# Kernel tuning notes

Measured on AMD Instinct MI355X. Metric: run time of the kernel, lower is better.

The kernel has to match this reference:

```python
import jax, jax.numpy as jnp
import numpy as np

N_NODES = 100000
N_EDGES = 1600000
DIM = 64
BN_EPS = 1e-5


def setup_inputs() -> dict:
    key = jax.random.key(0)
    ks = jax.random.split(key, 6)
    x = jax.random.normal(ks[0], (N_NODES, DIM), dtype=jnp.float32)
    edge_index = jax.random.randint(ks[1], (2, N_EDGES), 0, N_NODES, dtype=jnp.int32)
    W = jax.random.normal(ks[2], (DIM, DIM), dtype=jnp.float32) / np.sqrt(DIM)
    b = jax.random.normal(ks[3], (DIM,), dtype=jnp.float32) * 0.01
    gamma = jnp.ones((DIM,), dtype=jnp.float32)
    beta = jnp.zeros((DIM,), dtype=jnp.float32)
    return {"x": x, "edge_index": edge_index, "W": W, "b": b, "gamma": gamma, "beta": beta}


def reference(x, edge_index, W, b, gamma, beta):
    n = x.shape[0]
    src, dst = edge_index[0], edge_index[1]
    # GCNConv adds self loops
    loop = jnp.arange(n, dtype=edge_index.dtype)
    src = jnp.concatenate([src, loop])
    dst = jnp.concatenate([dst, loop])
    # symmetric degree normalization: D^-1/2 (A+I) D^-1/2
    deg = jax.ops.segment_sum(jnp.ones(src.shape[0], x.dtype), dst, num_segments=n)
    dinv = jnp.where(deg > 0, jax.lax.rsqrt(deg), 0.0)
    norm = dinv[src] * dinv[dst]  # [E+N]
    h = x @ W  # [N, D] transform before aggregation (GCN order)
    msg = h[src] * norm[:, None]  # gather + scale
    out = jax.ops.segment_sum(msg, dst, num_segments=n) + b  # scatter-add
    # BatchNorm1d (training mode: batch statistics, biased variance)
    mean = jnp.mean(out, axis=0)
    var = jnp.mean(jnp.square(out - mean), axis=0)
    out = (out - mean) * jax.lax.rsqrt(var + BN_EPS) * gamma + beta
    # ReLU; dropout is identity in eval mode
    return jax.nn.relu(out)
```

## Files before the change

### kernel.cpp

```cpp
#include <hip/hip_runtime.h>

#define N_NODES 100000
#define N_EDGES 1600000
#define DIM 64
#define BN_EPS 1e-5f

#define BNODES 128
#define NBUCK ((N_NODES + BNODES - 1) / BNODES)
#define CAP_RAW 2560
#define CAP_OUT 3584
#define TILE 8192
#define ABLK ((N_EDGES + TILE - 1) / TILE)

#define GBLK 6250
#define NREP 32

typedef __bf16 bf16x8 __attribute__((ext_vector_type(8)));
typedef float floatx4 __attribute__((ext_vector_type(4)));

static __device__ __forceinline__ unsigned short f2bf(float f) {
    unsigned u = __float_as_uint(f);
    u = (u + 0x7FFFu + ((u >> 16) & 1u)) >> 16;
    return (unsigned short)u;
}
static __device__ __forceinline__ float bf2f(unsigned short h) {
    return __uint_as_float(((unsigned)h) << 16);
}

__global__ void __launch_bounds__(1024)
passA_kernel(const int* __restrict__ src, const int* __restrict__ dst,
             int* __restrict__ cur, unsigned int* __restrict__ entries, int E) {
    __shared__ int hist[NBUCK];
    __shared__ int lbase[NBUCK];
    int t = threadIdx.x;
    if (t < NBUCK) hist[t] = 0;
    __syncthreads();

    int e0   = blockIdx.x * TILE;
    int eend = min(e0 + TILE, E);
    int eb   = e0 + t * 8;

    int dreg[8], sreg[8], ne = 0;
    if (eb + 7 < eend) {
        int4 d4 = *(const int4*)(dst + eb);
        int4 s4 = *(const int4*)(src + eb);
        int4 d5 = *(const int4*)(dst + eb + 4);
        int4 s5 = *(const int4*)(src + eb + 4);
        dreg[0] = d4.x; dreg[1] = d4.y; dreg[2] = d4.z; dreg[3] = d4.w;
        sreg[0] = s4.x; sreg[1] = s4.y; sreg[2] = s4.z; sreg[3] = s4.w;
        dreg[4] = d5.x; dreg[5] = d5.y; dreg[6] = d5.z; dreg[7] = d5.w;
        sreg[4] = s5.x; sreg[5] = s5.y; sreg[6] = s5.z; sreg[7] = s5.w;
        ne = 8;
    } else {
        for (int e = eb; e < eend && ne < 8; ++e, ++ne) {
            dreg[ne] = dst[e];
            sreg[ne] = src[e];
        }
    }
#pragma unroll
    for (int k = 0; k < 8; ++k)
        if (k < ne) atomicAdd(&hist[dreg[k] >> 7], 1);
    __syncthreads();
    if (t < NBUCK) {
        int ii = t + (blockIdx.x * 331) % NBUCK;
        if (ii >= NBUCK) ii -= NBUCK;
        int c = hist[ii];
        lbase[ii] = (c > 0) ? atomicAdd(&cur[ii], c) : 0;
        hist[ii] = 0;
    }
    __syncthreads();
#pragma unroll
    for (int k = 0; k < 8; ++k) {
        if (k >= ne) break;
        int s = sreg[k];
        int d = dreg[k];
        int b = d >> 7;
        int r = atomicAdd(&hist[b], 1);
        int pos = lbase[b] + r;
        if (pos < CAP_RAW)
            entries[(size_t)b * CAP_OUT + pos] = ((unsigned)s << 7) | (unsigned)(d & 127);
    }
}

__global__ void __launch_bounds__(256)
build_kernel(unsigned int* __restrict__ entries, const int* __restrict__ cur,
             int* __restrict__ rowbeg, int* __restrict__ rowend,
             float* __restrict__ dinv,
             const float* __restrict__ x, const float* __restrict__ W,
             unsigned short* __restrict__ hb, int dummyIdx, int N) {
    __shared__ int hist[BNODES * 4];
    __shared__ int nstart[BNODES];
    __shared__ int cursor[BNODES * 4];
    __shared__ int w0tot;
    int bucket = blockIdx.x;
    int t = threadIdx.x;
    int lane = t & 63, wv = t >> 6;
    int node0 = bucket * BNODES;
    int nn = min(BNODES, N - node0);
    int cnt = min(cur[bucket], CAP_RAW);
    unsigned int* eb = entries + (size_t)bucket * CAP_OUT;

    int m = lane & 15, quad = lane >> 4;
    int nchunk = nn >> 4;
    bool vA = (wv < nchunk);
    bool vB = (wv + 4 < nchunk);
    int rowA = node0 + wv * 16 + m;
    int rowB = node0 + (wv + 4) * 16 + m;
    float4 xA[4], xB[4];
    if (vA) {
        const float* xr = x + (size_t)rowA * DIM;
#pragma unroll
        for (int c = 0; c < 2; ++c) {
            xA[c * 2]     = *(const float4*)(xr + c * 32 + quad * 8);
            xA[c * 2 + 1] = *(const float4*)(xr + c * 32 + quad * 8 + 4);
        }
    }
    if (vB) {
        const float* xr = x + (size_t)rowB * DIM;
#pragma unroll
        for (int c = 0; c < 2; ++c) {
            xB[c * 2]     = *(const float4*)(xr + c * 32 + quad * 8);
            xB[c * 2 + 1] = *(const float4*)(xr + c * 32 + quad * 8 + 4);
        }
    }

    for (int i = t; i < BNODES * 4; i += 256) hist[i] = 0;
    __syncthreads();

    unsigned int ereg[10];
#pragma unroll
    for (int k = 0; k < 10; ++k) {
        int i = t + k * 256;
        if (i < cnt) {
            unsigned int e = eb[i];
            ereg[k] = e;
            int s = (int)(e >> 7);
            int q = (s >= 25000) + (s >= 50000) + (s >= 75000);
            atomicAdd(&hist[((e & 127) << 2) | q], 1);
        }
    }

    bf16x8 bfrag[2][4];
#pragma unroll
    for (int c = 0; c < 2; ++c)
#pragma unroll
        for (int nt = 0; nt < 4; ++nt) {
            bf16x8 f;
#pragma unroll
            for (int j = 0; j < 8; ++j) {
                int k = c * 32 + quad * 8 + j;
                f[j] = (__bf16)W[k * DIM + nt * 16 + m];
            }
            bfrag[c][nt] = f;
        }
    __syncthreads();

    int lrowA = wv * 16 + m, lrowB = (wv + 4) * 16 + m;
    float dvA = rsqrtf((float)(1 + hist[lrowA * 4] + hist[lrowA * 4 + 1] +
                               hist[lrowA * 4 + 2] + hist[lrowA * 4 + 3]));
    float dvB = rsqrtf((float)(1 + hist[lrowB * 4] + hist[lrowB * 4 + 1] +
                               hist[lrowB * 4 + 2] + hist[lrowB * 4 + 3]));

    int deg_t = 0, pdeg_t = 0;
    if (t < BNODES) {
        deg_t = hist[t * 4] + hist[t * 4 + 1] + hist[t * 4 + 2] + hist[t * 4 + 3];
        pdeg_t = (deg_t + 7) & ~7;
    }
    int v = pdeg_t;
#pragma unroll
    for (int off = 1; off < 64; off <<= 1) {
        int u = __shfl_up(v, off, 64);
        if (lane >= off) v += u;
    }
    if (t == 63) w0tot = v;
    __syncthreads();
    if (t < BNODES) {
        int incl = v + (wv == 1 ? w0tot : 0);
        int ex = incl - pdeg_t;
        nstart[t] = ex;
        int o = ex;
        cursor[t * 4 + 0] = o; o += hist[t * 4 + 0];
        cursor[t * 4 + 1] = o; o += hist[t * 4 + 1];
        cursor[t * 4 + 2] = o; o += hist[t * 4 + 2];
        cursor[t * 4 + 3] = o;
    }
    __syncthreads();
#pragma unroll
    for (int k = 0; k < 10; ++k) {
        int i = t + k * 256;
        if (i < cnt) {
            unsigned int e = ereg[k];
            int s = (int)(e >> 7);
            int q = (s >= 25000) + (s >= 50000) + (s >= 75000);
            int p = atomicAdd(&cursor[((e & 127) << 2) | q], 1);
            eb[p] = (unsigned)s;
        }
    }
    if (t < nn) {
        int dg  = deg_t;
        int pdg = pdeg_t;
        int base = nstart[t];
        for (int k = dg; k < pdg; ++k) eb[base + k] = (unsigned)dummyIdx;
        int gbase = bucket * CAP_OUT + base;
        rowbeg[node0 + t] = gbase;
        rowend[node0 + t] = gbase + pdg;
        dinv[node0 + t] = rsqrtf((float)(dg + 1));
    }

#pragma unroll
    for (int slot = 0; slot < 2; ++slot) {
        bool valid = slot == 0 ? vA : vB;
        if (!valid) continue;
        int row = slot == 0 ? rowA : rowB;
        float dv = slot == 0 ? dvA : dvB;
        bf16x8 afrag[2];
#pragma unroll
        for (int c = 0; c < 2; ++c) {
            float4 lo = slot == 0 ? xA[c * 2] : xB[c * 2];
            float4 hi = slot == 0 ? xA[c * 2 + 1] : xB[c * 2 + 1];
            bf16x8 f;
            f[0] = (__bf16)lo.x; f[1] = (__bf16)lo.y; f[2] = (__bf16)lo.z; f[3] = (__bf16)lo.w;
            f[4] = (__bf16)hi.x; f[5] = (__bf16)hi.y; f[6] = (__bf16)hi.z; f[7] = (__bf16)hi.w;
            afrag[c] = f;
        }
#pragma unroll
        for (int nt = 0; nt < 4; ++nt) {
            floatx4 acc = {0.f, 0.f, 0.f, 0.f};
            acc = __builtin_amdgcn_mfma_f32_16x16x32_bf16(bfrag[0][nt], afrag[0], acc, 0, 0, 0);
            acc = __builtin_amdgcn_mfma_f32_16x16x32_bf16(bfrag[1][nt], afrag[1], acc, 0, 0, 0);
            ushort4 pk;
            pk.x = f2bf(acc[0] * dv);
            pk.y = f2bf(acc[1] * dv);
            pk.z = f2bf(acc[2] * dv);
            pk.w = f2bf(acc[3] * dv);
            *(ushort4*)(hb + (size_t)row * DIM + nt * 16 + quad * 4) = pk;
        }
    }
}

__global__ void __launch_bounds__(256)
gather_kernel(const int* __restrict__ rowbeg, const int* __restrict__ rowend,
              const unsigned int* __restrict__ srt, const unsigned short* __restrict__ hb,
              const float* __restrict__ dinv, unsigned short* __restrict__ hbout,
              float* __restrict__ gstatRep, int N) {
    __shared__ float red[2][4][64];
    int lane = threadIdx.x & 63;
    int wv   = threadIdx.x >> 6;
    int g    = blockIdx.x * 4 + wv;
    int n0   = g << 2;
    float s_sum = 0.f, s_sq = 0.f;

    if (n0 < N) {
        int beg = __builtin_amdgcn_readfirstlane(rowbeg[n0]);
        int s1  = __builtin_amdgcn_readfirstlane(rowbeg[n0 + 1]);
        int s2  = __builtin_amdgcn_readfirstlane(rowbeg[n0 + 2]);
        int s3  = __builtin_amdgcn_readfirstlane(rowbeg[n0 + 3]);
        int end = __builtin_amdgcn_readfirstlane(rowend[n0 + 3]);
        float acc0 = 0.f, acc1 = 0.f, acc2 = 0.f, acc3 = 0.f;

        unsigned int sv = (beg + lane < end) ? srt[beg + lane] : 0u;
        for (int base = beg; base < end; base += 64) {
            int nidx = base + 64 + lane;
            unsigned int sv_next = (nidx < end) ? srt[nidx] : 0u;
            int cn = min(64, end - base);
            int j = 0;
            for (; j + 16 <= cn; j += 16) {
                int pA = base + j;
                int pB = pA + 8;
                int kA = (pA >= s1) + (pA >= s2) + (pA >= s3);
                int kB = (pB >= s1) + (pB >= s2) + (pB >= s3);
                float v[16];
#pragma unroll
                for (int u = 0; u < 16; ++u) {
                    unsigned int s = (unsigned)__builtin_amdgcn_readlane((int)sv, j + u);
                    v[u] = bf2f(hb[(size_t)s * DIM + lane]);
                }
                float cA = ((v[0] + v[1]) + (v[2] + v[3])) +
                           ((v[4] + v[5]) + (v[6] + v[7]));
                float cB = ((v[8] + v[9]) + (v[10] + v[11])) +
                           ((v[12] + v[13]) + (v[14] + v[15]));
                acc0 += (kA == 0) ? cA : 0.f;
                acc1 += (kA == 1) ? cA : 0.f;
                acc2 += (kA == 2) ? cA : 0.f;
                acc3 += (kA == 3) ? cA : 0.f;
                acc0 += (kB == 0) ? cB : 0.f;
                acc1 += (kB == 1) ? cB : 0.f;
                acc2 += (kB == 2) ? cB : 0.f;
                acc3 += (kB == 3) ? cB : 0.f;
            }
            for (; j < cn; j += 8) {
                int p0 = base + j;
                int k = (p0 >= s1) + (p0 >= s2) + (p0 >= s3);
                float v[8];
#pragma unroll
                for (int u = 0; u < 8; ++u) {
                    unsigned int s = (unsigned)__builtin_amdgcn_readlane((int)sv, j + u);
                    v[u] = bf2f(hb[(size_t)s * DIM + lane]);
                }
                float csum = ((v[0] + v[1]) + (v[2] + v[3])) +
                             ((v[4] + v[5]) + (v[6] + v[7]));
                acc0 += (k == 0) ? csum : 0.f;
                acc1 += (k == 1) ? csum : 0.f;
                acc2 += (k == 2) ? csum : 0.f;
                acc3 += (k == 3) ? csum : 0.f;
            }
            sv = sv_next;
        }

        float v0 = (acc0 + bf2f(hb[(size_t)(n0 + 0) * DIM + lane])) * dinv[n0 + 0];
        float v1 = (acc1 + bf2f(hb[(size_t)(n0 + 1) * DIM + lane])) * dinv[n0 + 1];
        float v2 = (acc2 + bf2f(hb[(size_t)(n0 + 2) * DIM + lane])) * dinv[n0 + 2];
        float v3 = (acc3 + bf2f(hb[(size_t)(n0 + 3) * DIM + lane])) * dinv[n0 + 3];
        unsigned short r0 = f2bf(v0), r1 = f2bf(v1), r2 = f2bf(v2), r3 = f2bf(v3);
        hbout[(size_t)(n0 + 0) * DIM + lane] = r0;
        hbout[(size_t)(n0 + 1) * DIM + lane] = r1;
        hbout[(size_t)(n0 + 2) * DIM + lane] = r2;
        hbout[(size_t)(n0 + 3) * DIM + lane] = r3;
        float w0 = bf2f(r0), w1 = bf2f(r1), w2 = bf2f(r2), w3 = bf2f(r3);
        s_sum = ((w0 + w1) + (w2 + w3));
        s_sq  = ((w0 * w0 + w1 * w1) + (w2 * w2 + w3 * w3));
    }

    red[0][wv][lane] = s_sum;
    red[1][wv][lane] = s_sq;
    __syncthreads();
    if (threadIdx.x < 128) {
        int c = threadIdx.x & 63;
        int which = threadIdx.x >> 6;
        float v = red[which][0][c] + red[which][1][c] + red[which][2][c] + red[which][3][c];
        float* dst = gstatRep + (size_t)(blockIdx.x & (NREP - 1)) * 128 + which * 64 + c;
        atomicAdd(dst, v);
    }
}

__global__ void __launch_bounds__(256)
finish_kernel(const ushort4* __restrict__ hbo, float4* __restrict__ out,
              const float* __restrict__ gstatRep,
              const float* __restrict__ gamma, const float* __restrict__ beta,
              int total4, int N) {
    __shared__ float scale[64];
    __shared__ float shift[64];
    __shared__ float stat[128];
    int t = threadIdx.x;
    if (t < 128) {
        int c = t & 63;
        int which = t >> 6;
        float acc = 0.f;
#pragma unroll
        for (int r = 0; r < NREP; ++r)
            acc += gstatRep[(size_t)r * 128 + which * 64 + c];
        stat[t] = acc;
    }
    __syncthreads();
    if (t < 64) {
        float invN = 1.0f / (float)N;
        float mean = stat[t] * invN;
        float var  = stat[64 + t] * invN - mean * mean;
        float sc   = gamma[t] * rsqrtf(var + BN_EPS);
        scale[t] = sc;
        shift[t] = beta[t] - mean * sc;
    }
    __syncthreads();
    int i = blockIdx.x * blockDim.x + t;
    if (i >= total4) return;
    int c = (i * 4) & 63;
    ushort4 u = hbo[i];
    float4 v;
    float a0 = fmaf(bf2f(u.x), scale[c],     shift[c]);
    float a1 = fmaf(bf2f(u.y), scale[c + 1], shift[c + 1]);
    float a2 = fmaf(bf2f(u.z), scale[c + 2], shift[c + 2]);
    float a3 = fmaf(bf2f(u.w), scale[c + 3], shift[c + 3]);
    v.x = a0 > 0.f ? a0 : 0.f;
    v.y = a1 > 0.f ? a1 : 0.f;
    v.z = a2 > 0.f ? a2 : 0.f;
    v.w = a3 > 0.f ? a3 : 0.f;
    out[i] = v;
}

extern "C" void kernel_launch(void* const* d_in, const int* in_sizes, int n_in,
                              void* d_out, int out_size, void* d_ws, size_t ws_size,
                              hipStream_t stream) {
    const float* x     = (const float*)d_in[0];
    const int*   eidx  = (const int*)d_in[1];
    const float* W     = (const float*)d_in[2];
    const float* gamma = (const float*)d_in[4];
    const float* beta  = (const float*)d_in[5];
    float* out = (float*)d_out;

    const int N = N_NODES;
    const int total = N * DIM;

    const int* src = eidx;
    const int* dst = eidx + N_EDGES;

    char* ws = (char*)d_ws;
    size_t off_hb      = 0;
    size_t off_hbout   = off_hb + (size_t)N * DIM * 2;
    size_t off_dinv    = off_hbout + (size_t)N * DIM * 2;
    size_t off_rowbeg  = off_dinv + (size_t)N * 4;
    size_t off_rowend  = off_rowbeg + (size_t)N * 4;
    size_t off_entries = off_rowend + (size_t)N * 4;
    size_t off_z       = off_entries + (size_t)NBUCK * CAP_OUT * 4;

    unsigned short* hb     = (unsigned short*)(ws + off_hb);
    unsigned short* hbout  = (unsigned short*)(ws + off_hbout);
    float*          dinv   = (float*)(ws + off_dinv);
    int*            rowbeg = (int*)(ws + off_rowbeg);
    int*            rowend = (int*)(ws + off_rowend);
    unsigned int*   entries = (unsigned int*)(ws + off_entries);
    int*   cur      = (int*)(ws + off_z + 128);
    float* gstatRep = (float*)(cur + NBUCK);
    int dummyIdx = (int)(off_z / (DIM * 2));

    size_t zbytes = 128 + (size_t)NBUCK * 4 + (size_t)NREP * 128 * 4;
    hipMemsetAsync(ws + off_z, 0, zbytes, stream);

    passA_kernel<<<ABLK, 1024, 0, stream>>>(src, dst, cur, entries, N_EDGES);

    build_kernel<<<NBUCK, 256, 0, stream>>>(entries, cur, rowbeg, rowend, dinv,
                                            x, W, hb, dummyIdx, N);

    gather_kernel<<<GBLK, 256, 0, stream>>>(rowbeg, rowend, entries, hb, dinv,
                                            hbout, gstatRep, N);

    finish_kernel<<<(total / 4 + 255) / 256, 256, 0, stream>>>((const ushort4*)hbout,
                                                               (float4*)out, gstatRep,
                                                               gamma, beta, total / 4, N);
}
```

Measured before the change: 166.5 us.

## Stage bucketed edges in shared memory for coalesced global writes

```diff
diff --git a/kernel.cpp b/kernel.cpp
--- a/kernel.cpp
+++ b/kernel.cpp
@@ -31,8 +31,13 @@
 passA_kernel(const int* __restrict__ src, const int* __restrict__ dst,
              int* __restrict__ cur, unsigned int* __restrict__ entries, int E) {
     __shared__ int hist[NBUCK];
-    __shared__ int lbase[NBUCK];
+    __shared__ int lstart[NBUCK];
+    __shared__ int lcur[NBUCK];
+    __shared__ int gbase[NBUCK];
+    __shared__ int wtot[16];
+    __shared__ unsigned int stage[TILE];
     int t = threadIdx.x;
+    int lane = t & 63, wv = t >> 6;
     if (t < NBUCK) hist[t] = 0;
     __syncthreads();
 
@@ -61,24 +66,55 @@
     for (int k = 0; k < 8; ++k)
         if (k < ne) atomicAdd(&hist[dreg[k] >> 7], 1);
     __syncthreads();
+
     if (t < NBUCK) {
         int ii = t + (blockIdx.x * 331) % NBUCK;
         if (ii >= NBUCK) ii -= NBUCK;
         int c = hist[ii];
-        lbase[ii] = (c > 0) ? atomicAdd(&cur[ii], c) : 0;
-        hist[ii] = 0;
-    }
-    __syncthreads();
+        gbase[ii] = (c > 0) ? atomicAdd(&cur[ii], c) : 0;
+    }
+
+    int val = (t < NBUCK) ? hist[t] : 0;
+    int incl = val;
+#pragma unroll
+    for (int off = 1; off < 64; off <<= 1) {
+        int u = __shfl_up(incl, off, 64);
+        if (lane >= off) incl += u;
+    }
+    if (lane == 63) wtot[wv] = incl;
+    __syncthreads();
+    if (t == 0) {
+        int run = 0;
+#pragma unroll
+        for (int i = 0; i < 16; ++i) { int c = wtot[i]; wtot[i] = run; run += c; }
+    }
+    __syncthreads();
+    if (t < NBUCK) {
+        int ls = incl - val + wtot[wv];
+        lstart[t] = ls;
+        lcur[t] = ls;
+    }
+    __syncthreads();
+
 #pragma unroll
     for (int k = 0; k < 8; ++k) {
         if (k >= ne) break;
         int s = sreg[k];
         int d = dreg[k];
         int b = d >> 7;
-        int r = atomicAdd(&hist[b], 1);
-        int pos = lbase[b] + r;
-        if (pos < CAP_RAW)
-            entries[(size_t)b * CAP_OUT + pos] = ((unsigned)s << 7) | (unsigned)(d & 127);
+        int p = atomicAdd(&lcur[b], 1);
+        stage[p] = ((unsigned)s << 7) | (unsigned)(d & 127);
+    }
+    __syncthreads();
+
+    for (int b = wv; b < NBUCK; b += 16) {
+        int ls  = lstart[b];
+        int cnt = hist[b];
+        int gb  = gbase[b];
+        unsigned int* dstp = entries + (size_t)b * CAP_OUT + gb;
+        for (int o = lane; o < cnt; o += 64)
+            if (gb + o < CAP_RAW)
+                dstp[o] = stage[ls + o];
     }
 }
 
```

Result: no change. 169.0 us (+1.4%).
